# Optimization experiments

Hardware: AMD Instinct MI355X
Metric: run time of the kernel (lower is better)

Reference implementation:

```python
import jax, jax.numpy as jnp
import numpy as np

B, L, DM, DI, N = 8, 2048, 512, 768, 8  # batch, seq, d_model, d_inner=int(1.5*512), d_state


def setup_inputs() -> dict:
    key = jax.random.key(0)
    ks = jax.random.split(key, 8)
    g = lambda k, shape, sc=1.0: (jax.random.normal(k, shape, jnp.float32) * sc)
    return {
        "x": g(ks[0], (B, L, DM)),
        "W_in": g(ks[1], (DM, 2 * DI), 0.02),    # in_proj weight (stored in->out)
        "A_log": g(ks[2], (DI, N)),               # nn.Parameter(randn)
        "D_param": g(ks[3], (DI,)),               # skip-connection D
        "W_x": g(ks[4], (DI, N), 0.02),           # x_proj weight
        "W_dt": g(ks[5], (N, DI), 0.02),          # dt_proj weight
        "b_dt": jnp.zeros((DI,), jnp.float32),    # dt_proj bias
        "W_out": g(ks[6], (DI, DM), 0.02),        # out_proj weight
    }


def reference(x, W_in, A_log, D_param, W_x, W_dt, b_dt, W_out):
    xz = x @ W_in                                  # (B,L,2*DI)
    d_inner = W_in.shape[1] // 2
    x_ssm, z = xz[..., :d_inner], xz[..., d_inner:]
    x_ssm = jax.nn.silu(x_ssm)                     # (B,L,DI)
    A = -jnp.exp(A_log.astype(jnp.float32))        # (DI,N)
    delta = jax.nn.softplus((x_ssm @ W_x) @ W_dt + b_dt)  # (B,L,DI)

    n_state = A.shape[-1]

    def step(h, inp):
        xt, dt = inp                               # each (B,DI)
        dA = jnp.exp(dt[..., None] * A)            # (B,DI,N)
        h = dA * h + dt[..., None] * xt[..., None]
        y = jnp.sum(h, axis=-1) + D_param * xt     # (B,DI)
        return h, y

    h0 = jnp.zeros((x.shape[0], d_inner, n_state), x_ssm.dtype)
    xs = (jnp.swapaxes(x_ssm, 0, 1), jnp.swapaxes(delta, 0, 1))  # (L,B,DI)
    _, ys = jax.lax.scan(step, h0, xs)             # ys: (L,B,DI)
    y = jnp.swapaxes(ys, 0, 1)                     # (B,L,DI)
    y = y * jax.nn.silu(z)
    return y @ W_out                               # (B,L,DM)
```

## Files before the change

### kernel.cpp

```cpp
#include <hip/hip_runtime.h>

typedef unsigned short bfu;
typedef __attribute__((ext_vector_type(8))) short short8;
typedef __attribute__((ext_vector_type(4))) float f32x4;

__device__ __forceinline__ float bf2f(bfu u){
  union { unsigned int i; float f; } v; v.i = ((unsigned int)u) << 16; return v.f;
}
__device__ __forceinline__ bfu f2bf(float f){
  union { float f; unsigned int i; } v; v.f = f;
  unsigned int r = (v.i + 0x7FFFu + ((v.i >> 16) & 1u)) >> 16;
  return (bfu)r;
}
__device__ __forceinline__ float fexp2(float x){ return __builtin_amdgcn_exp2f(x); }
__device__ __forceinline__ float flog2(float x){ return __builtin_amdgcn_logf(x); }
__device__ __forceinline__ float softplusf(float x){
  float t = fexp2(-fabsf(x) * 1.44269504088896f);
  return fmaxf(x, 0.f) + 0.69314718055995f * flog2(1.f + t);
}
__device__ __forceinline__ void gload16(const bfu* g, bfu* l){
  __builtin_amdgcn_global_load_lds((const __attribute__((address_space(1))) unsigned int*)g,
                                   (__attribute__((address_space(3))) unsigned int*)l, 16, 0, 0);
}

__global__ __launch_bounds__(256) void cvt4_kernel(const float* __restrict__ in, bfu* __restrict__ out, int n4){
  int g = blockIdx.x * 256 + threadIdx.x;
  if (g < n4){
    float4 v = ((const float4*)in)[g];
    ushort4 o;
    o.x = f2bf(v.x); o.y = f2bf(v.y); o.z = f2bf(v.z); o.w = f2bf(v.w);
    ((ushort4*)out)[g] = o;
  }
}

__global__ __launch_bounds__(256) void cvtT2_kernel(const float* __restrict__ W_in, const float* __restrict__ W_out,
                                                    const float* __restrict__ W_x,
                                                    bfu* __restrict__ WinT, bfu* __restrict__ WoutT,
                                                    float* __restrict__ WxT){
  int g = blockIdx.x * 256 + threadIdx.x;
  if (g < 786432){
    int r = g % 512, c = g / 512;
    WinT[g] = f2bf(W_in[(size_t)r * 1536 + c]);
  } else if (g < 786432 + 393216){
    int h = g - 786432;
    int r = h % 768, c = h / 768;
    WoutT[h] = f2bf(W_out[(size_t)r * 512 + c]);
  } else if (g < 786432 + 393216 + 6144){
    int h = g - (786432 + 393216);
    int n = h / 768, k = h % 768;
    WxT[h] = W_x[(size_t)k * 8 + n];
  }
}

template<int EPI>
__global__ __launch_bounds__(512)
void gemm_big(const bfu* __restrict__ Amat, const bfu* __restrict__ Bt,
              void* __restrict__ out0, void* __restrict__ out1,
              int NBN, int N, int K)
{
  __shared__ bfu As[256 * 64];
  __shared__ bfu Bs[128 * 64];
  const int tid  = threadIdx.x;
  const int lane = tid & 63;
  const int w    = tid >> 6;
  const int wr   = w >> 1, wc = w & 1;

  const int cpx = gridDim.x >> 3;
  const int id  = blockIdx.x;
  const int nid = (id & 7) * cpx + (id >> 3);
  const int bn  = nid % NBN;
  const int bm  = nid / NBN;

  const int srow = tid >> 3;
  const int scol = ((tid & 7) ^ (srow & 7)) * 8;
  const bfu* gA = Amat + ((size_t)(bm * 256 + srow)) * K + scol;
  const bfu* gB = Bt   + ((size_t)(bn * 128 + srow)) * K + scol;
  bfu* lA = As + srow * 64 + (tid & 7) * 8;
  bfu* lB = Bs + srow * 64 + (tid & 7) * 8;

  f32x4 acc[4][4];
  #pragma unroll
  for (int i = 0; i < 4; i++)
    #pragma unroll
    for (int j = 0; j < 4; j++)
      #pragma unroll
      for (int r = 0; r < 4; r++) acc[i][j][r] = 0.f;

  for (int k0 = 0; k0 < K; k0 += 64){
    #pragma unroll
    for (int i = 0; i < 4; i++)
      gload16(gA + (size_t)(i * 64) * K + k0, lA + i * 64 * 64);
    #pragma unroll
    for (int i = 0; i < 2; i++)
      gload16(gB + (size_t)(i * 64) * K + k0, lB + i * 64 * 64);
    __syncthreads();

    #pragma unroll
    for (int kk = 0; kk < 2; kk++){
      short8 a[4], b[4];
      const int sA = ((kk * 4 + (lane >> 4)) ^ (lane & 7)) * 8;
      #pragma unroll
      for (int m = 0; m < 4; m++){
        int r = wr * 64 + m * 16 + (lane & 15);
        a[m] = *(const short8*)&As[r * 64 + sA];
      }
      #pragma unroll
      for (int n = 0; n < 4; n++){
        int r = wc * 64 + n * 16 + (lane & 15);
        b[n] = *(const short8*)&Bs[r * 64 + sA];
      }
      #pragma unroll
      for (int m = 0; m < 4; m++)
        #pragma unroll
        for (int n = 0; n < 4; n++)
          acc[m][n] = __builtin_amdgcn_mfma_f32_16x16x32_bf16(a[m], b[n], acc[m][n], 0, 0, 0);
    }
    __syncthreads();
  }

  #pragma unroll
  for (int m = 0; m < 4; m++){
    #pragma unroll
    for (int n = 0; n < 4; n++){
      const int row0 = bm * 256 + wr * 64 + m * 16 + (lane >> 4) * 4;
      const int col  = bn * 128 + wc * 64 + n * 16 + (lane & 15);
      #pragma unroll
      for (int r = 0; r < 4; r++){
        float v = acc[m][n][r];
        int row = row0 + r;
        if (EPI == 0){
          float s = v / (1.f + __expf(-v));
          if (col < 768) ((bfu*)out0)[(size_t)row * 768 + col]         = f2bf(s);
          else           ((bfu*)out1)[(size_t)row * 768 + (col - 768)] = f2bf(s);
        } else {
          ((float*)out0)[(size_t)row * N + col] = v;
        }
      }
    }
  }
}

__global__ __launch_bounds__(256) void u_kernel(const bfu* __restrict__ xssm, const float* __restrict__ WxT,
                                                float* __restrict__ u){
  int wid = threadIdx.x >> 6, lane = threadIdx.x & 63;
  int row = blockIdx.x * 4 + wid;
  const bfu* xr = xssm + (size_t)row * 768;
  float acc[8];
  #pragma unroll
  for (int n = 0; n < 8; n++) acc[n] = 0.f;
  #pragma unroll
  for (int i = 0; i < 3; i++){
    int kb = i * 256 + lane * 4;
    ushort4 xq = *(const ushort4*)(xr + kb);
    float x0 = bf2f(xq.x), x1 = bf2f(xq.y), x2 = bf2f(xq.z), x3 = bf2f(xq.w);
    #pragma unroll
    for (int n = 0; n < 8; n++){
      float4 wv = *(const float4*)(WxT + (size_t)n * 768 + kb);
      acc[n] += x0 * wv.x + x1 * wv.y + x2 * wv.z + x3 * wv.w;
    }
  }
  #pragma unroll
  for (int n = 0; n < 8; n++){
    #pragma unroll
    for (int off = 32; off >= 1; off >>= 1) acc[n] += __shfl_xor(acc[n], off, 64);
  }
  if (lane == 0){
    float4 o0 = { acc[0], acc[1], acc[2], acc[3] };
    float4 o1 = { acc[4], acc[5], acc[6], acc[7] };
    *(float4*)(u + (size_t)row * 8)     = o0;
    *(float4*)(u + (size_t)row * 8 + 4) = o1;
  }
}

__global__ __launch_bounds__(128) void scan_phase1(const bfu* __restrict__ xssm, const float* __restrict__ u,
    const float* __restrict__ Wdt, const float* __restrict__ bdt, const float* __restrict__ A_log,
    float* __restrict__ Pws, float* __restrict__ Hws){
  int tid = threadIdx.x;
  int bid = blockIdx.x;
  int b = bid / 192; int rem = bid % 192;
  int c = rem / 3;   int dblk = rem % 3;
  int d0 = dblk * 256 + tid * 2;
  float Al2[2][8], H[2][8], Wr[2][8], bd[2], S[2];
  #pragma unroll
  for (int j = 0; j < 2; j++){
    bd[j] = bdt[d0 + j];
    S[j] = 0.f;
    #pragma unroll
    for (int n = 0; n < 8; n++){
      Al2[j][n] = -__expf(A_log[(size_t)(d0 + j) * 8 + n]) * 1.4426950408889634f;
      Wr[j][n]  = Wdt[(size_t)n * 768 + d0 + j];
      H[j][n] = 0.f;
    }
  }
  int r0 = b * 2048 + c * 32;
  size_t base = (size_t)r0 * 768 + d0;
  #pragma unroll 8
  for (int i = 0; i < 32; i++){
    float4 u0 = *(const float4*)(u + (size_t)(r0 + i) * 8);
    float4 u1 = *(const float4*)(u + (size_t)(r0 + i) * 8 + 4);
    ushort2 xq = *(const ushort2*)(xssm + base + (size_t)i * 768);
    #pragma unroll
    for (int j = 0; j < 2; j++){
      float xt = bf2f(j == 0 ? xq.x : xq.y);
      float dv = bd[j] + u0.x * Wr[j][0] + u0.y * Wr[j][1] + u0.z * Wr[j][2] + u0.w * Wr[j][3]
                       + u1.x * Wr[j][4] + u1.y * Wr[j][5] + u1.z * Wr[j][6] + u1.w * Wr[j][7];
      float dt = softplusf(dv);
      float dx = dt * xt;
      S[j] += dt;
      #pragma unroll
      for (int n = 0; n < 8; n++){
        float e = fexp2(dt * Al2[j][n]);
        H[j][n] = e * H[j][n] + dx;
      }
    }
  }
  size_t o = (((size_t)b * 64 + c) * 768 + d0) * 8;
  #pragma unroll
  for (int j = 0; j < 2; j++){
    float4 p0, p1;
    p0.x = fexp2(S[j] * Al2[j][0]); p0.y = fexp2(S[j] * Al2[j][1]);
    p0.z = fexp2(S[j] * Al2[j][2]); p0.w = fexp2(S[j] * Al2[j][3]);
    p1.x = fexp2(S[j] * Al2[j][4]); p1.y = fexp2(S[j] * Al2[j][5]);
    p1.z = fexp2(S[j] * Al2[j][6]); p1.w = fexp2(S[j] * Al2[j][7]);
    float4 h0 = { H[j][0], H[j][1], H[j][2], H[j][3] };
    float4 h1 = { H[j][4], H[j][5], H[j][6], H[j][7] };
    *(float4*)(Pws + o + j * 8)     = p0;
    *(float4*)(Pws + o + j * 8 + 4) = p1;
    *(float4*)(Hws + o + j * 8)     = h0;
    *(float4*)(Hws + o + j * 8 + 4) = h1;
  }
}

__global__ __launch_bounds__(256) void scan_phase2(float* __restrict__ Pws, const float* __restrict__ Hws){
  int g = blockIdx.x * 256 + threadIdx.x;
  int within = g % 6144;
  int b = g / 6144;
  size_t base = (size_t)b * 64 * 6144 + within;
  float hin = 0.f;
  #pragma unroll 8
  for (int c = 0; c < 64; c++){
    size_t idx = base + (size_t)c * 6144;
    float p = Pws[idx], hh = Hws[idx];
    Pws[idx] = hin;
    hin = p * hin + hh;
  }
}

__global__ __launch_bounds__(128) void scan_phase3(const bfu* __restrict__ xssm, const float* __restrict__ u,
    const float* __restrict__ Wdt, const float* __restrict__ bdt, const float* __restrict__ A_log,
    const float* __restrict__ Dp, const bfu* __restrict__ siluz, const float* __restrict__ Hin,
    bfu* __restrict__ yz){
  int tid = threadIdx.x;
  int bid = blockIdx.x;
  int b = bid / 192; int rem = bid % 192;
  int c = rem / 3;   int dblk = rem % 3;
  int d0 = dblk * 256 + tid * 2;
  float Al2[2][8], H[2][8], Wr[2][8], bd[2], Dd[2];
  size_t o = (((size_t)b * 64 + c) * 768 + d0) * 8;
  #pragma unroll
  for (int j = 0; j < 2; j++){
    bd[j] = bdt[d0 + j];
    Dd[j] = Dp[d0 + j];
    float4 h0 = *(const float4*)(Hin + o + j * 8);
    float4 h1 = *(const float4*)(Hin + o + j * 8 + 4);
    H[j][0] = h0.x; H[j][1] = h0.y; H[j][2] = h0.z; H[j][3] = h0.w;
    H[j][4] = h1.x; H[j][5] = h1.y; H[j][6] = h1.z; H[j][7] = h1.w;
    #pragma unroll
    for (int n = 0; n < 8; n++){
      Al2[j][n] = -__expf(A_log[(size_t)(d0 + j) * 8 + n]) * 1.4426950408889634f;
      Wr[j][n]  = Wdt[(size_t)n * 768 + d0 + j];
    }
  }
  int r0 = b * 2048 + c * 32;
  size_t base = (size_t)r0 * 768 + d0;
  #pragma unroll 8
  for (int i = 0; i < 32; i++){
    float4 u0 = *(const float4*)(u + (size_t)(r0 + i) * 8);
    float4 u1 = *(const float4*)(u + (size_t)(r0 + i) * 8 + 4);
    ushort2 xq = *(const ushort2*)(xssm + base + (size_t)i * 768);
    ushort2 zq = *(const ushort2*)(siluz + base + (size_t)i * 768);
    ushort2 oq;
    #pragma unroll
    for (int j = 0; j < 2; j++){
      float xt = bf2f(j == 0 ? xq.x : xq.y);
      float dv = bd[j] + u0.x * Wr[j][0] + u0.y * Wr[j][1] + u0.z * Wr[j][2] + u0.w * Wr[j][3]
                       + u1.x * Wr[j][4] + u1.y * Wr[j][5] + u1.z * Wr[j][6] + u1.w * Wr[j][7];
      float dt = softplusf(dv);
      float dx = dt * xt;
      float y = Dd[j] * xt;
      #pragma unroll
      for (int n = 0; n < 8; n++){
        float e = fexp2(dt * Al2[j][n]);
        H[j][n] = e * H[j][n] + dx;
        y += H[j][n];
      }
      float sz = bf2f(j == 0 ? zq.x : zq.y);
      bfu r = f2bf(y * sz);
      if (j == 0) oq.x = r; else oq.y = r;
    }
    *(ushort2*)(yz + base + (size_t)i * 768) = oq;
  }
}

extern "C" void kernel_launch(void* const* d_in, const int* in_sizes, int n_in,
                              void* d_out, int out_size, void* d_ws, size_t ws_size,
                              hipStream_t stream){
  const float* x     = (const float*)d_in[0];
  const float* W_in  = (const float*)d_in[1];
  const float* A_log = (const float*)d_in[2];
  const float* D_par = (const float*)d_in[3];
  const float* W_x   = (const float*)d_in[4];
  const float* W_dt  = (const float*)d_in[5];
  const float* b_dt  = (const float*)d_in[6];
  const float* W_out = (const float*)d_in[7];
  float* out = (float*)d_out;
  (void)in_sizes; (void)n_in; (void)out_size; (void)ws_size;

  char* base = (char*)d_ws;
  size_t off = 0;
  auto alloc = [&](size_t bytes)->char*{
    char* p = base + off; off += (bytes + 255) & ~(size_t)255; return p;
  };
  bfu*   x_bf  = (bfu*)  alloc((size_t)16384 * 512 * 2);
  bfu*   WinT  = (bfu*)  alloc((size_t)1536 * 512 * 2);
  bfu*   WoutT = (bfu*)  alloc((size_t)512 * 768 * 2);
  float* WxT   = (float*)alloc((size_t)8 * 768 * 4);
  bfu*   xssm  = (bfu*)  alloc((size_t)16384 * 768 * 2);
  bfu*   siluz = (bfu*)  alloc((size_t)16384 * 768 * 2);
  float* u     = (float*)alloc((size_t)16384 * 8 * 4);
  float* Pws   = (float*)alloc((size_t)8 * 64 * 768 * 8 * 4);
  float* Hws   = (float*)alloc((size_t)8 * 64 * 768 * 8 * 4);
  bfu*   yz    = (bfu*)  alloc((size_t)16384 * 768 * 2);

  cvt4_kernel<<<8192, 256, 0, stream>>>(x, x_bf, 2097152);
  cvtT2_kernel<<<4632, 256, 0, stream>>>(W_in, W_out, W_x, WinT, WoutT, WxT);
  gemm_big<0><<<768, 512, 0, stream>>>(x_bf, WinT, xssm, siluz, 12, 1536, 512);
  u_kernel<<<4096, 256, 0, stream>>>(xssm, WxT, u);
  scan_phase1<<<1536, 128, 0, stream>>>(xssm, u, W_dt, b_dt, A_log, Pws, Hws);
  scan_phase2<<<192, 256, 0, stream>>>(Pws, Hws);
  scan_phase3<<<1536, 128, 0, stream>>>(xssm, u, W_dt, b_dt, A_log, D_par, siluz, Pws, yz);
  gemm_big<1><<<256, 512, 0, stream>>>(yz, WoutT, out, nullptr, 4, 512, 768);
}
```

Before: 170.6 us.

## Double-buffer GEMM LDS tiles with 128x128 blocks and merge conversion kernels

Replaces the 256x128, 512-thread GEMM with a 128x128, 256-thread version that keeps two LDS stages. The next K-tile's global-to-LDS loads are issued before computing on the current tile, with explicit vmcnt waits and barriers, so memory latency can overlap MFMA work. K becomes a compile-time constant so the loop fully unrolls, and MFMA sections run at raised wave priority. The two fp32-to-bf16 conversion kernels are merged into one launch; the cost is smaller tiles with more blocks and reliance on hand-written waitcnt ordering.

```diff
diff --git a/kernel.cpp b/kernel.cpp
--- a/kernel.cpp
+++ b/kernel.cpp
@@ -23,43 +23,43 @@
                                    (__attribute__((address_space(3))) unsigned int*)l, 16, 0, 0);
 }
 
-__global__ __launch_bounds__(256) void cvt4_kernel(const float* __restrict__ in, bfu* __restrict__ out, int n4){
+__global__ __launch_bounds__(256) void cvt_all_kernel(const float* __restrict__ x, bfu* __restrict__ x_bf,
+                                                      const float* __restrict__ W_in, const float* __restrict__ W_out,
+                                                      const float* __restrict__ W_x,
+                                                      bfu* __restrict__ WinT, bfu* __restrict__ WoutT,
+                                                      float* __restrict__ WxT){
   int g = blockIdx.x * 256 + threadIdx.x;
-  if (g < n4){
-    float4 v = ((const float4*)in)[g];
+  if (g < 2097152){
+    float4 v = ((const float4*)x)[g];
     ushort4 o;
     o.x = f2bf(v.x); o.y = f2bf(v.y); o.z = f2bf(v.z); o.w = f2bf(v.w);
-    ((ushort4*)out)[g] = o;
-  }
-}
-
-__global__ __launch_bounds__(256) void cvtT2_kernel(const float* __restrict__ W_in, const float* __restrict__ W_out,
-                                                    const float* __restrict__ W_x,
-                                                    bfu* __restrict__ WinT, bfu* __restrict__ WoutT,
-                                                    float* __restrict__ WxT){
-  int g = blockIdx.x * 256 + threadIdx.x;
-  if (g < 786432){
-    int r = g % 512, c = g / 512;
-    WinT[g] = f2bf(W_in[(size_t)r * 1536 + c]);
-  } else if (g < 786432 + 393216){
-    int h = g - 786432;
-    int r = h % 768, c = h / 768;
-    WoutT[h] = f2bf(W_out[(size_t)r * 512 + c]);
-  } else if (g < 786432 + 393216 + 6144){
-    int h = g - (786432 + 393216);
-    int n = h / 768, k = h % 768;
-    WxT[h] = W_x[(size_t)k * 8 + n];
-  }
-}
-
-template<int EPI>
-__global__ __launch_bounds__(512)
-void gemm_big(const bfu* __restrict__ Amat, const bfu* __restrict__ Bt,
-              void* __restrict__ out0, void* __restrict__ out1,
-              int NBN, int N, int K)
+    ((ushort4*)x_bf)[g] = o;
+    return;
+  }
+  int h = g - 2097152;
+  if (h < 786432){
+    int r = h % 512, c = h / 512;
+    WinT[h] = f2bf(W_in[(size_t)r * 1536 + c]);
+  } else if (h < 786432 + 393216){
+    int h2 = h - 786432;
+    int r = h2 % 768, c = h2 / 768;
+    WoutT[h2] = f2bf(W_out[(size_t)r * 512 + c]);
+  } else if (h < 786432 + 393216 + 6144){
+    int h2 = h - (786432 + 393216);
+    int n = h2 / 768, k = h2 % 768;
+    WxT[h2] = W_x[(size_t)k * 8 + n];
+  }
+}
+
+template<int EPI, int KK>
+__global__ __launch_bounds__(256)
+void gemm_db(const bfu* __restrict__ Amat, const bfu* __restrict__ Bt,
+             void* __restrict__ out0, void* __restrict__ out1,
+             int NBN, int N)
 {
-  __shared__ bfu As[256 * 64];
-  __shared__ bfu Bs[128 * 64];
+  constexpr int NT = KK / 64;
+  __shared__ bfu As[2 * 128 * 64];
+  __shared__ bfu Bs[2 * 128 * 64];
   const int tid  = threadIdx.x;
   const int lane = tid & 63;
   const int w    = tid >> 6;
@@ -73,10 +73,19 @@
 
   const int srow = tid >> 3;
   const int scol = ((tid & 7) ^ (srow & 7)) * 8;
-  const bfu* gA = Amat + ((size_t)(bm * 256 + srow)) * K + scol;
-  const bfu* gB = Bt   + ((size_t)(bn * 128 + srow)) * K + scol;
-  bfu* lA = As + srow * 64 + (tid & 7) * 8;
-  bfu* lB = Bs + srow * 64 + (tid & 7) * 8;
+  const bfu* gA = Amat + ((size_t)(bm * 128 + srow)) * KK + scol;
+  const bfu* gB = Bt   + ((size_t)(bn * 128 + srow)) * KK + scol;
+  bfu* lA = As + tid * 8;
+  bfu* lB = Bs + tid * 8;
+
+  auto STAGE = [&](int t, int sel){
+    const int k0 = t * 64;
+    #pragma unroll
+    for (int i = 0; i < 4; i++){
+      gload16(gA + (size_t)(i * 32) * KK + k0, lA + sel * 8192 + i * 2048);
+      gload16(gB + (size_t)(i * 32) * KK + k0, lB + sel * 8192 + i * 2048);
+    }
+  };
 
   f32x4 acc[4][4];
   #pragma unroll
@@ -86,15 +95,17 @@
       #pragma unroll
       for (int r = 0; r < 4; r++) acc[i][j][r] = 0.f;
 
-  for (int k0 = 0; k0 < K; k0 += 64){
-    #pragma unroll
-    for (int i = 0; i < 4; i++)
-      gload16(gA + (size_t)(i * 64) * K + k0, lA + i * 64 * 64);
-    #pragma unroll
-    for (int i = 0; i < 2; i++)
-      gload16(gB + (size_t)(i * 64) * K + k0, lB + i * 64 * 64);
-    __syncthreads();
-
+  STAGE(0, 0);
+  STAGE(1, 1);
+
+  #pragma unroll
+  for (int t = 0; t < NT; ++t){
+    if (t + 1 < NT) asm volatile("s_waitcnt vmcnt(8)" ::: "memory");
+    else            asm volatile("s_waitcnt vmcnt(0)" ::: "memory");
+    __builtin_amdgcn_s_barrier();
+
+    const bfu* Ab = As + (t & 1) * 8192;
+    const bfu* Bb = Bs + (t & 1) * 8192;
     #pragma unroll
     for (int kk = 0; kk < 2; kk++){
       short8 a[4], b[4];
@@ -102,27 +113,30 @@
       #pragma unroll
       for (int m = 0; m < 4; m++){
         int r = wr * 64 + m * 16 + (lane & 15);
-        a[m] = *(const short8*)&As[r * 64 + sA];
+        a[m] = *(const short8*)&Ab[r * 64 + sA];
       }
       #pragma unroll
       for (int n = 0; n < 4; n++){
         int r = wc * 64 + n * 16 + (lane & 15);
-        b[n] = *(const short8*)&Bs[r * 64 + sA];
-      }
+        b[n] = *(const short8*)&Bb[r * 64 + sA];
+      }
+      __builtin_amdgcn_s_setprio(1);
       #pragma unroll
       for (int m = 0; m < 4; m++)
         #pragma unroll
         for (int n = 0; n < 4; n++)
           acc[m][n] = __builtin_amdgcn_mfma_f32_16x16x32_bf16(a[m], b[n], acc[m][n], 0, 0, 0);
-    }
-    __syncthreads();
+      __builtin_amdgcn_s_setprio(0);
+    }
+    __builtin_amdgcn_s_barrier();
+    if (t + 2 < NT) STAGE(t + 2, t & 1);
   }
 
   #pragma unroll
   for (int m = 0; m < 4; m++){
     #pragma unroll
     for (int n = 0; n < 4; n++){
-      const int row0 = bm * 256 + wr * 64 + m * 16 + (lane >> 4) * 4;
+      const int row0 = bm * 128 + wr * 64 + m * 16 + (lane >> 4) * 4;
       const int col  = bn * 128 + wc * 64 + n * 16 + (lane & 15);
       #pragma unroll
       for (int r = 0; r < 4; r++){
@@ -332,12 +346,11 @@
   float* Hws   = (float*)alloc((size_t)8 * 64 * 768 * 8 * 4);
   bfu*   yz    = (bfu*)  alloc((size_t)16384 * 768 * 2);
 
-  cvt4_kernel<<<8192, 256, 0, stream>>>(x, x_bf, 2097152);
-  cvtT2_kernel<<<4632, 256, 0, stream>>>(W_in, W_out, W_x, WinT, WoutT, WxT);
-  gemm_big<0><<<768, 512, 0, stream>>>(x_bf, WinT, xssm, siluz, 12, 1536, 512);
+  cvt_all_kernel<<<12824, 256, 0, stream>>>(x, x_bf, W_in, W_out, W_x, WinT, WoutT, WxT);
+  gemm_db<0, 512><<<1536, 256, 0, stream>>>(x_bf, WinT, xssm, siluz, 12, 1536);
   u_kernel<<<4096, 256, 0, stream>>>(xssm, WxT, u);
   scan_phase1<<<1536, 128, 0, stream>>>(xssm, u, W_dt, b_dt, A_log, Pws, Hws);
   scan_phase2<<<192, 256, 0, stream>>>(Pws, Hws);
   scan_phase3<<<1536, 128, 0, stream>>>(xssm, u, W_dt, b_dt, A_log, D_par, siluz, Pws, yz);
-  gemm_big<1><<<256, 512, 0, stream>>>(yz, WoutT, out, nullptr, 4, 512, 768);
-}
+  gemm_db<1, 768><<<512, 256, 0, stream>>>(yz, WoutT, out, nullptr, 4, 512);
+}
```

Result: no change. 168.5 us (-1.2%).
